# Performance work log

Measured on AMD Instinct MI355X. Metric: run time of the kernel, lower is better.

The kernel has to match this reference:

```python
import jax, jax.numpy as jnp
import numpy as np

IN_DIM = 128
OUT_DIM = 128
EDGE_DIM = 64
NUM_HEADS = 8
HEAD_DIM = OUT_DIM // NUM_HEADS
N_NODES = 10000
N_EDGES = 320000
LN_EPS = 1e-5


def _gelu(x):
    # torch nn.GELU default is the exact (erf) formulation
    return jax.nn.gelu(x, approximate=False)


def _layernorm(x, g, b):
    mu = jnp.mean(x, axis=-1, keepdims=True)
    var = jnp.var(x, axis=-1, keepdims=True)
    return (x - mu) * jax.lax.rsqrt(var + LN_EPS) * g + b


def setup_inputs() -> dict:
    key = jax.random.key(0)
    ks = jax.random.split(key, 16)

    def lin(k, fan_in, fan_out):
        # torch nn.Linear default init: U(-1/sqrt(fan_in), 1/sqrt(fan_in))
        bound = 1.0 / np.sqrt(fan_in)
        kw, kb = jax.random.split(k)
        w = jax.random.uniform(kw, (fan_in, fan_out), jnp.float32, -bound, bound)
        b = jax.random.uniform(kb, (fan_out,), jnp.float32, -bound, bound)
        return w, b

    node_features = jax.random.normal(ks[0], (N_NODES, IN_DIM), jnp.float32)
    edge_index = jax.random.randint(ks[1], (2, N_EDGES), 0, N_NODES)
    edge_attr = jax.random.normal(ks[2], (N_EDGES, EDGE_DIM), jnp.float32)

    msg_w1, msg_b1 = lin(ks[3], 2 * IN_DIM + EDGE_DIM, OUT_DIM)
    msg_w2, msg_b2 = lin(ks[4], OUT_DIM, OUT_DIM)
    q_w, q_b = lin(ks[5], IN_DIM, OUT_DIM)
    kv_w, kv_b = lin(ks[6], IN_DIM + EDGE_DIM, OUT_DIM)
    out_w1, out_b1 = lin(ks[7], IN_DIM + OUT_DIM, OUT_DIM)
    out_w2, out_b2 = lin(ks[8], OUT_DIM, OUT_DIM)
    ln_g = 1.0 + 0.02 * jax.random.normal(ks[9], (OUT_DIM,), jnp.float32)
    ln_b = 0.02 * jax.random.normal(ks[10], (OUT_DIM,), jnp.float32)

    return dict(node_features=node_features, edge_attr=edge_attr,
                msg_w1=msg_w1, msg_b1=msg_b1, msg_w2=msg_w2, msg_b2=msg_b2,
                q_w=q_w, q_b=q_b, kv_w=kv_w, kv_b=kv_b,
                out_w1=out_w1, out_b1=out_b1, out_w2=out_w2, out_b2=out_b2,
                ln_g=ln_g, ln_b=ln_b, edge_index=edge_index)


def reference(node_features, edge_attr, msg_w1, msg_b1, msg_w2, msg_b2,
              q_w, q_b, kv_w, kv_b, out_w1, out_b1, out_w2, out_b2,
              ln_g, ln_b, edge_index):
    N = node_features.shape[0]
    E = edge_index.shape[1]
    src, dst = edge_index[0], edge_index[1]

    s = node_features[src]                      # [E, Din]
    d = node_features[dst]                      # [E, Din]

    # message MLP
    m_in = jnp.concatenate([s, d, edge_attr], axis=-1)          # [E, 2*Din+De]
    m = _gelu(m_in @ msg_w1 + msg_b1) @ msg_w2 + msg_b2         # [E, Dout]

    # per-edge attention logits
    q = (d @ q_w + q_b).reshape(E, NUM_HEADS, HEAD_DIM)
    kv_in = jnp.concatenate([s, edge_attr], axis=-1)
    kv = (kv_in @ kv_w + kv_b).reshape(E, NUM_HEADS, HEAD_DIM)
    attn = jnp.sum(q * kv, axis=-1) * (HEAD_DIM ** -0.5)        # [E, H]

    # Deterministic version: pick the edge with the largest index per dst node.
    last = jnp.full((N,), -1, dtype=jnp.int32).at[dst].max(
        jnp.arange(E, dtype=jnp.int32))                          # [N]
    attn_full = jnp.where(last[:, None] >= 0,
                          attn[jnp.maximum(last, 0)],
                          -jnp.inf)                              # [N, H]
    # softmax over the NODE axis (dim=0), exactly as the torch code does;
    # -inf rows contribute 0, so using N instead of dst.max()+1 is identical.
    attn_norm = jax.nn.softmax(attn_full, axis=0)[dst]           # [E, H]

    m = (m.reshape(E, NUM_HEADS, HEAD_DIM) * attn_norm[..., None]).reshape(E, OUT_DIM)

    # scatter-add aggregation
    agg = jax.ops.segment_sum(m, dst, num_segments=N)            # [N, Dout]

    h_in = jnp.concatenate([node_features, agg], axis=-1)        # [N, Din+Dout]
    h = _gelu(h_in @ out_w1 + out_b1) @ out_w2 + out_b2          # [N, Dout]

    # res_proj is Identity since in_dim == out_dim; dropout is eval-mode no-op
    return _layernorm(node_features + h, ln_g, ln_b)
```

## Files before the change

### kernel.cpp

```cpp
#include <hip/hip_runtime.h>
#include <hip/hip_bf16.h>

#define NN 10000
#define NE 320000

typedef __bf16 bf16x8 __attribute__((ext_vector_type(8)));
typedef float  f32x4  __attribute__((ext_vector_type(4)));

__device__ __forceinline__ float bf2f(ushort u){
  union { uint i; float f; } c; c.i = ((uint)u) << 16; return c.f;
}
__device__ __forceinline__ ushort f2bf(float f){
  union { float f; uint i; } c; c.f = f;
  uint x = c.i;
  return (ushort)((x + 0x7FFFu + ((x >> 16) & 1u)) >> 16);
}
__device__ __forceinline__ float gelu_erf(float x){
  return 0.5f * x * (1.0f + erff(x * 0.70710678118654752f));
}
__device__ __forceinline__ float gelu_tanh(float x){
  float y = 0.7978845608028654f * (x + 0.044715f * x * x * x);
  float e = __expf(2.f * y);
  float th = 1.f - 2.f / (e + 1.f);
  return 0.5f * x * (1.f + th);
}
__device__ __forceinline__ uint encf(float f){
  uint u = __float_as_uint(f);
  return (u & 0x80000000u) ? ~u : (u | 0x80000000u);
}
__device__ __forceinline__ float decf(uint u){
  return __uint_as_float((u & 0x80000000u) ? (u & 0x7FFFFFFFu) : ~u);
}
#define MFMA16(a,b,c) __builtin_amdgcn_mfma_f32_16x16x32_bf16((a),(b),(c),0,0,0)

__global__ void k_init(const uint* __restrict__ w, int* __restrict__ flag,
                       int* __restrict__ cnt, int* __restrict__ last,
                       uint* __restrict__ Menc, float* __restrict__ S){
  int t = threadIdx.x;
  if (blockIdx.x == 0){
    uint c = 0;
    for (int i = t; i < 4096; i += 256){
      uint v = w[i * 63];
      uint e = (v >> 7) & 0xFF;
      if (e >= 100 && e <= 140) c++;
    }
    __shared__ uint red[256];
    red[t] = c; __syncthreads();
    for (int s = 128; s > 0; s >>= 1){
      if (t < s) red[t] += red[t + s];
      __syncthreads();
    }
    if (t == 0) *flag = (red[0] < 2048) ? 1 : 0;
    return;
  }
  int idx = (blockIdx.x - 1) * 256 + t;
  if (idx < 10000) last[idx] = -1;
  else if (idx < 20000) cnt[idx - 10000] = 0;
  else if (idx < 20008) Menc[idx - 20000] = 0u;
  else if (idx < 20016) S[idx - 20008] = 0.f;
}

__global__ void k_prep(
    const void* NF0, const int* __restrict__ dstI,
    const void* w1, const void* w2, const void* qw, const void* kvw,
    const void* ow1, const void* ow2,
    const void* b1, const void* b2, const void* qb, const void* kvb,
    const void* ob1, const void* ob2, const void* lg, const void* lb,
    int* __restrict__ cnt, int* __restrict__ last,
    ushort* NFc, float* Gagg, ushort* SB, ushort* KVW2,
    ushort* W1aT, ushort* W1bT, ushort* W1cT, ushort* W2T, ushort* QT, ushort* KVT,
    ushort* O1aT, ushort* O1bT, ushort* O2T, const int* flag)
{
  int f = *flag;
  int idx = blockIdx.x * 256 + threadIdx.x;
  if (idx < NE){
    int d = dstI[idx];
    atomicAdd(&cnt[d], 1);
    atomicMax(&last[d], idx);
    return;
  }
  idx -= NE;
  if (idx < 320000){
    if (f){
      float4 v = ((const float4*)NF0)[idx];
      ushort4 o; o.x=f2bf(v.x); o.y=f2bf(v.y); o.z=f2bf(v.z); o.w=f2bf(v.w);
      ((ushort4*)NFc)[idx] = o;
    } else ((ushort4*)NFc)[idx] = ((const ushort4*)NF0)[idx];
    return;
  }
  idx -= 320000;
  if (idx < 320000){ float4 z = {0.f,0.f,0.f,0.f}; ((float4*)Gagg)[idx] = z; return; }
  idx -= 320000;
  if (idx < 1024){
    const void* ps[8] = {b1,b2,qb,kvb,ob1,ob2,lg,lb};
    const void* p = ps[idx >> 7]; int j = idx & 127;
    SB[idx] = f ? f2bf(((const float*)p)[j]) : ((const ushort*)p)[j];
    return;
  }
  idx -= 1024;
  if (idx < 8192){
    KVW2[idx] = f ? f2bf(((const float*)kvw)[16384 + idx]) : ((const ushort*)kvw)[16384 + idx];
    return;
  }
  idx -= 8192;
  if (idx < 16384){ int c=idx>>7,k=idx&127; W1aT[idx] = f? f2bf(((const float*)w1)[k*128+c]) : ((const ushort*)w1)[k*128+c]; return; }
  idx -= 16384;
  if (idx < 16384){ int c=idx>>7,k=idx&127; W1bT[idx] = f? f2bf(((const float*)w1)[(128+k)*128+c]) : ((const ushort*)w1)[(128+k)*128+c]; return; }
  idx -= 16384;
  if (idx < 8192){ int c=idx>>6,k=idx&63;  W1cT[idx] = f? f2bf(((const float*)w1)[(256+k)*128+c]) : ((const ushort*)w1)[(256+k)*128+c]; return; }
  idx -= 8192;
  if (idx < 16384){ int c=idx>>7,k=idx&127; W2T[idx] = f? f2bf(((const float*)w2)[k*128+c]) : ((const ushort*)w2)[k*128+c]; return; }
  idx -= 16384;
  if (idx < 16384){ int c=idx>>7,k=idx&127; QT[idx]  = f? f2bf(((const float*)qw)[k*128+c]) : ((const ushort*)qw)[k*128+c]; return; }
  idx -= 16384;
  if (idx < 16384){ int c=idx>>7,k=idx&127; KVT[idx] = f? f2bf(((const float*)kvw)[k*128+c]) : ((const ushort*)kvw)[k*128+c]; return; }
  idx -= 16384;
  if (idx < 16384){ int c=idx>>7,k=idx&127; O1aT[idx] = f? f2bf(((const float*)ow1)[k*128+c]) : ((const ushort*)ow1)[k*128+c]; return; }
  idx -= 16384;
  if (idx < 16384){ int c=idx>>7,k=idx&127; O1bT[idx] = f? f2bf(((const float*)ow1)[(128+k)*128+c]) : ((const ushort*)ow1)[(128+k)*128+c]; return; }
  idx -= 16384;
  if (idx < 16384){ int c=idx>>7,k=idx&127; O2T[idx] = f? f2bf(((const float*)ow2)[k*128+c]) : ((const ushort*)ow2)[k*128+c]; return; }
}

__global__ __launch_bounds__(1024) void k_scan(const int* __restrict__ cnt,
                                               int* __restrict__ fill){
  __shared__ int sc[1024];
  int t = threadIdx.x;
  int base = t * 10;
  int v[10]; int tot = 0;
  #pragma unroll
  for (int j = 0; j < 10; ++j){
    int idx = base + j;
    v[j] = (idx < NN) ? cnt[idx] : 0;
    tot += v[j];
  }
  sc[t] = tot; __syncthreads();
  for (int off = 1; off < 1024; off <<= 1){
    int x = (t >= off) ? sc[t - off] : 0;
    __syncthreads();
    sc[t] += x;
    __syncthreads();
  }
  int run = sc[t] - tot;
  #pragma unroll
  for (int j = 0; j < 10; ++j){
    int idx = base + j;
    if (idx < NN) fill[idx] = run;
    run += v[j];
  }
}

__global__ __launch_bounds__(256) void k_fillperm(
    const int* __restrict__ srcI, const int* __restrict__ dstI,
    int* __restrict__ fill, int* __restrict__ sSort, int* __restrict__ dSort,
    int* __restrict__ eSort,
    const ushort* __restrict__ NFc,
    const ushort* __restrict__ W1aT, const ushort* __restrict__ W1bT,
    const ushort* __restrict__ QT,  const ushort* __restrict__ KVT,
    const ushort* __restrict__ SB,
    ushort* __restrict__ PA, ushort* __restrict__ PB,
    ushort* __restrict__ Qb, ushort* __restrict__ KV1)
{
  int t = threadIdx.x;
  if (blockIdx.x >= 1250){
    int l = t & 63, w = t >> 6;
    int m = l & 15, g = l >> 4;
    int row0 = ((int)blockIdx.x - 1250) * 16;
    const ushort* WT = (w==0) ? W1aT : (w==1) ? W1bT : (w==2) ? QT : KVT;
    ushort*       OUT= (w==0) ? PA   : (w==1) ? PB   : (w==2) ? Qb : KV1;
    const f32x4 FZ = {0.f,0.f,0.f,0.f};
    f32x4 acc[8];
    #pragma unroll
    for (int i = 0; i < 8; ++i) acc[i] = FZ;
    int arow = row0 + m;
    #pragma unroll
    for (int ks = 0; ks < 4; ++ks){
      int koff = ks * 32 + g * 8;
      bf16x8 a = *reinterpret_cast<const bf16x8*>(NFc + (size_t)arow * 128 + koff);
      #pragma unroll
      for (int nt = 0; nt < 8; ++nt){
        bf16x8 b = *reinterpret_cast<const bf16x8*>(WT + (size_t)(nt*16+m) * 128 + koff);
        acc[nt] = MFMA16(a, b, acc[nt]);
      }
    }
    #pragma unroll
    for (int nt = 0; nt < 8; ++nt){
      int col = nt * 16 + m;
      float bb = (w==1) ? bf2f(SB[col]) : (w==2) ? bf2f(SB[256+col]) : (w==3) ? bf2f(SB[384+col]) : 0.f;
      #pragma unroll
      for (int r = 0; r < 4; ++r){
        int row = row0 + g * 4 + r;
        OUT[(size_t)row * 128 + col] = f2bf(acc[nt][r] + bb);
      }
    }
    return;
  }
  int e = blockIdx.x * 256 + t;
  int d = dstI[e];
  int p = atomicAdd(&fill[d], 1);
  sSort[p] = srcI[e];
  dSort[p] = d;
  eSort[p] = e;
}

__global__ __launch_bounds__(256) void k_edgeattn(
    const ushort* __restrict__ PA, const ushort* __restrict__ PB,
    const int* __restrict__ sSort, const int* __restrict__ dSort,
    const int* __restrict__ eSort,
    const ushort* __restrict__ W1cT,
    float* __restrict__ Gagg,
    const ushort* __restrict__ Qb, const ushort* __restrict__ KV1,
    const ushort* __restrict__ EAb, const float* __restrict__ EAf,
    const ushort* __restrict__ KVW2,
    const int* __restrict__ srcI, const int* __restrict__ last,
    float* __restrict__ attn, uint* __restrict__ Menc, const int* __restrict__ flag)
{
  __shared__ __align__(16) char Hs[64 * 256];
  __shared__ __align__(16) char EAl[64 * 128];
  __shared__ int sIdx[64], dIdx[64], eIdx[64];
  __shared__ int eN[16], sN[16];
  __shared__ uint lmax[8];
  int t = threadIdx.x;

  if (blockIdx.x >= 5000){
    float (*ea_s)[64] = reinterpret_cast<float(*)[64]>(Hs);
    int n0 = ((int)blockIdx.x - 5000) * 16;
    if (t < 16){
      int e = last[n0 + t];
      eN[t] = e;
      sN[t] = (e >= 0) ? srcI[e] : 0;
    }
    if (t < 8) lmax[t] = 0u;
    __syncthreads();
    int F = *flag;
    for (int i = t; i < 1024; i += 256){
      int nn = i >> 6, k = i & 63;
      int e = eN[nn];
      int ee = (e >= 0) ? e : 0;
      float v = F ? EAf[(size_t)ee * 64 + k] : bf2f(EAb[(size_t)ee * 64 + k]);
      ea_s[nn][k] = (e >= 0) ? v : 0.0f;
    }
    __syncthreads();
    int j = t & 127;
    int half = t >> 7;
    float acc[8];
    #pragma unroll
    for (int i = 0; i < 8; ++i) acc[i] = 0.f;
    for (int k = 0; k < 64; ++k){
      float wv = bf2f(KVW2[(size_t)k * 128 + j]);
      #pragma unroll
      for (int nn = 0; nn < 8; ++nn) acc[nn] += ea_s[half * 8 + nn][k] * wv;
    }
    #pragma unroll
    for (int nn = 0; nn < 8; ++nn){
      int nl = half * 8 + nn;
      int n = n0 + nl;
      int e = eN[nl];
      float kvv = acc[nn] + bf2f(KV1[(size_t)sN[nl] * 128 + j]);
      float qv  = bf2f(Qb[(size_t)n * 128 + j]);
      float p = qv * kvv;
      p += __shfl_xor(p, 1); p += __shfl_xor(p, 2);
      p += __shfl_xor(p, 4); p += __shfl_xor(p, 8);
      if ((j & 15) == 0 && e >= 0){
        float v = p * 0.25f;
        attn[(size_t)n * 8 + (j >> 4)] = v;
        atomicMax(&lmax[j >> 4], encf(v));
      }
    }
    __syncthreads();
    if (t < 8 && lmax[t]) atomicMax(&Menc[t], lmax[t]);
    return;
  }

  int p0 = blockIdx.x * 64;
  int l = t & 63, w = t >> 6;
  int m = l & 15, g = l >> 4;

  if (t < 64){ sIdx[t] = sSort[p0 + t]; dIdx[t] = dSort[p0 + t]; eIdx[t] = eSort[p0 + t]; }
  __syncthreads();
  int F = *flag;

  {
    int r = t >> 2, q = t & 3;
    int e = eIdx[r];
    int kb = q * 32;
    if (F){
      const float* src = EAf + (size_t)e * 64 + q * 16;
      float4 v0 = *reinterpret_cast<const float4*>(src);
      float4 v1 = *reinterpret_cast<const float4*>(src + 4);
      float4 v2 = *reinterpret_cast<const float4*>(src + 8);
      float4 v3 = *reinterpret_cast<const float4*>(src + 12);
      bf16x8 o0, o1;
      o0[0]=(__bf16)v0.x; o0[1]=(__bf16)v0.y; o0[2]=(__bf16)v0.z; o0[3]=(__bf16)v0.w;
      o0[4]=(__bf16)v1.x; o0[5]=(__bf16)v1.y; o0[6]=(__bf16)v1.z; o0[7]=(__bf16)v1.w;
      o1[0]=(__bf16)v2.x; o1[1]=(__bf16)v2.y; o1[2]=(__bf16)v2.z; o1[3]=(__bf16)v2.w;
      o1[4]=(__bf16)v3.x; o1[5]=(__bf16)v3.y; o1[6]=(__bf16)v3.z; o1[7]=(__bf16)v3.w;
      *reinterpret_cast<bf16x8*>(&EAl[(r * 128 + kb)      ^ ((r & 7) << 4)]) = o0;
      *reinterpret_cast<bf16x8*>(&EAl[(r * 128 + kb + 16) ^ ((r & 7) << 4)]) = o1;
    } else {
      const ushort* src = EAb + (size_t)e * 64 + q * 16;
      *reinterpret_cast<bf16x8*>(&EAl[(r * 128 + kb)      ^ ((r & 7) << 4)]) =
        *reinterpret_cast<const bf16x8*>(src);
      *reinterpret_cast<bf16x8*>(&EAl[(r * 128 + kb + 16) ^ ((r & 7) << 4)]) =
        *reinterpret_cast<const bf16x8*>(src + 8);
    }
    int sr = sIdx[r], dr = dIdx[r];
    #pragma unroll
    for (int j = 0; j < 4; ++j){
      int c8 = q * 4 + j;
      bf16x8 pa = *reinterpret_cast<const bf16x8*>(PA + (size_t)sr * 128 + c8 * 8);
      bf16x8 pb = *reinterpret_cast<const bf16x8*>(PB + (size_t)dr * 128 + c8 * 8);
      bf16x8 ps;
      #pragma unroll
      for (int k = 0; k < 8; ++k) ps[k] = (__bf16)((float)pa[k] + (float)pb[k]);
      int byte = (r * 256 + c8 * 16) ^ ((r & 7) << 4);
      *reinterpret_cast<bf16x8*>(&Hs[byte]) = ps;
    }
  }
  __syncthreads();

  const f32x4 FZ = {0.f,0.f,0.f,0.f};
  f32x4 acc[8];
  #pragma unroll
  for (int i = 0; i < 8; ++i) acc[i] = FZ;

  #pragma unroll
  for (int ks = 0; ks < 2; ++ks){
    int row = w * 16 + m;
    bf16x8 af = *reinterpret_cast<const bf16x8*>(&EAl[(row * 128 + ks * 64 + g * 16) ^ ((row & 7) << 4)]);
    #pragma unroll
    for (int nt = 0; nt < 8; ++nt){
      bf16x8 b = *reinterpret_cast<const bf16x8*>(W1cT + (size_t)(nt * 16 + m) * 64 + ks * 32 + g * 8);
      acc[nt] = MFMA16(af, b, acc[nt]);
    }
  }

  #pragma unroll
  for (int nt = 0; nt < 8; ++nt){
    int col = nt * 16 + m;
    #pragma unroll
    for (int r = 0; r < 4; ++r){
      int row = w * 16 + g * 4 + r;
      int byte = (row * 256 + col * 2) ^ ((row & 7) << 4);
      float x = acc[nt][r] + bf2f(*reinterpret_cast<const ushort*>(&Hs[byte]));
      *reinterpret_cast<ushort*>(&Hs[byte]) = f2bf(gelu_tanh(x));
    }
  }
  __syncthreads();

  {
    int c = t & 127, hh = t >> 7;
    int rS = hh * 32, rE = rS + 32;
    float run = 0.f;
    int cur = dIdx[rS];
    for (int r = rS; r < rE; ++r){
      int d = dIdx[r];
      if (d != cur){
        unsafeAtomicAdd(&Gagg[(size_t)cur * 128 + c], run);
        run = 0.f; cur = d;
      }
      int byte = (r * 256 + c * 2) ^ ((r & 7) << 4);
      run += bf2f(*reinterpret_cast<const ushort*>(&Hs[byte]));
    }
    unsafeAtomicAdd(&Gagg[(size_t)cur * 128 + c], run);
  }
}

__global__ __launch_bounds__(256) void k_asum(
    const float* __restrict__ attn, const int* __restrict__ last,
    const uint* __restrict__ Menc, float* __restrict__ S)
{
  __shared__ float red[256][8];
  int t = threadIdx.x;
  float M[8];
  #pragma unroll
  for (int h = 0; h < 8; ++h) M[h] = decf(Menc[h]);
  float p[8];
  #pragma unroll
  for (int h = 0; h < 8; ++h) p[h] = 0.f;
  for (int n = blockIdx.x * 256 + t; n < NN; n += gridDim.x * 256){
    if (last[n] >= 0){
      #pragma unroll
      for (int h = 0; h < 8; ++h) p[h] += __expf(attn[(size_t)n * 8 + h] - M[h]);
    }
  }
  #pragma unroll
  for (int h = 0; h < 8; ++h) red[t][h] = p[h];
  __syncthreads();
  for (int s = 128; s > 0; s >>= 1){
    if (t < s){
      #pragma unroll
      for (int h = 0; h < 8; ++h) red[t][h] += red[t + s][h];
    }
    __syncthreads();
  }
  if (t < 8) atomicAdd(&S[t], red[0][t]);
}

__global__ __launch_bounds__(256) void k_aggmm2(
    const float* __restrict__ Gagg, const ushort* __restrict__ W2T,
    const ushort* __restrict__ O1aT, const ushort* __restrict__ O1bT,
    const ushort* __restrict__ SB,
    const int* __restrict__ cnt, const int* __restrict__ last,
    const float* __restrict__ attn, const uint* __restrict__ Menc,
    const float* __restrict__ S,
    const ushort* __restrict__ NFc, ushort* __restrict__ T1)
{
  __shared__ __align__(16) char Zs[64 * 256];
  int t = threadIdx.x, l = t & 63, w = t >> 6;
  int m = l & 15, g = l >> 4;
  int row0 = blockIdx.x * 64 + w * 16;

  float M[8], Sinv[8];
  #pragma unroll
  for (int h = 0; h < 8; ++h){ M[h] = decf(Menc[h]); Sinv[h] = 1.0f / S[h]; }

  int arow = row0 + m; if (arow >= NN) arow = NN - 1;
  const f32x4 FZ = {0.f,0.f,0.f,0.f};
  f32x4 acc[8];
  #pragma unroll
  for (int i = 0; i < 8; ++i) acc[i] = FZ;

  #pragma unroll
  for (int ks = 0; ks < 4; ++ks){
    const float* gp = Gagg + (size_t)arow * 128 + ks * 32 + g * 8;
    float4 u0 = *reinterpret_cast<const float4*>(gp);
    float4 u1 = *reinterpret_cast<const float4*>(gp + 4);
    float gv[8] = {u0.x,u0.y,u0.z,u0.w,u1.x,u1.y,u1.z,u1.w};
    bf16x8 hi, lo;
    #pragma unroll
    for (int k = 0; k < 8; ++k){
      hi[k] = (__bf16)gv[k];
      lo[k] = (__bf16)(gv[k] - (float)hi[k]);
    }
    #pragma unroll
    for (int nt = 0; nt < 8; ++nt){
      bf16x8 b = *reinterpret_cast<const bf16x8*>(W2T + (size_t)(nt*16+m) * 128 + ks * 32 + g * 8);
      acc[nt] = MFMA16(hi, b, acc[nt]);
      acc[nt] = MFMA16(lo, b, acc[nt]);
    }
  }

  #pragma unroll
  for (int r = 0; r < 4; ++r){
    int row = row0 + g * 4 + r;
    int rr = (row < NN) ? row : NN - 1;
    float cn = (float)cnt[rr];
    int lst = last[rr];
    int Lr = w * 16 + g * 4 + r;
    #pragma unroll
    for (int nt = 0; nt < 8; ++nt){
      int col = nt * 16 + m;
      float aw = (lst >= 0) ? __expf(attn[(size_t)rr * 8 + nt] - M[nt]) * Sinv[nt] : 0.f;
      float z = (acc[nt][r] + cn * bf2f(SB[128 + col])) * aw;
      int byte = (Lr * 256 + col * 2) ^ ((Lr & 7) << 4);
      *reinterpret_cast<ushort*>(&Zs[byte]) = f2bf(z);
    }
  }
  __syncthreads();

  f32x4 acc2[8];
  #pragma unroll
  for (int i = 0; i < 8; ++i) acc2[i] = FZ;
  int La = w * 16 + m;
  #pragma unroll
  for (int ks = 0; ks < 4; ++ks){
    int koff = ks * 32 + g * 8;
    bf16x8 az = *reinterpret_cast<const bf16x8*>(&Zs[(La * 256 + koff * 2) ^ ((La & 7) << 4)]);
    bf16x8 an = *reinterpret_cast<const bf16x8*>(NFc + (size_t)arow * 128 + koff);
    #pragma unroll
    for (int nt = 0; nt < 8; ++nt){
      bf16x8 b1v = *reinterpret_cast<const bf16x8*>(O1bT + (size_t)(nt*16+m) * 128 + koff);
      bf16x8 b2v = *reinterpret_cast<const bf16x8*>(O1aT + (size_t)(nt*16+m) * 128 + koff);
      acc2[nt] = MFMA16(az, b1v, acc2[nt]);
      acc2[nt] = MFMA16(an, b2v, acc2[nt]);
    }
  }
  #pragma unroll
  for (int nt = 0; nt < 8; ++nt){
    int col = nt * 16 + m;
    float bb = bf2f(SB[512 + col]);
    #pragma unroll
    for (int r = 0; r < 4; ++r){
      int row = row0 + g * 4 + r;
      if (row < NN){
        float v = gelu_erf(acc2[nt][r] + bb);
        T1[(size_t)row * 128 + col] = f2bf(v);
      }
    }
  }
}

__global__ __launch_bounds__(256) void k_out2ln(
    const ushort* __restrict__ T1, const ushort* __restrict__ O2T,
    const ushort* __restrict__ SB,
    const ushort* __restrict__ NFc, void* __restrict__ out,
    const int* __restrict__ flag)
{
  int t = threadIdx.x, l = t & 63, w = t >> 6;
  int m = l & 15, g = l >> 4;
  int row0 = blockIdx.x * 64 + w * 16;
  int F = *flag;
  int arow = row0 + m; if (arow >= NN) arow = NN - 1;
  const f32x4 FZ = {0.f,0.f,0.f,0.f};
  f32x4 acc[8];
  #pragma unroll
  for (int i = 0; i < 8; ++i) acc[i] = FZ;
  #pragma unroll
  for (int ks = 0; ks < 4; ++ks){
    int koff = ks * 32 + g * 8;
    bf16x8 a = *reinterpret_cast<const bf16x8*>(T1 + (size_t)arow * 128 + koff);
    #pragma unroll
    for (int nt = 0; nt < 8; ++nt){
      bf16x8 b = *reinterpret_cast<const bf16x8*>(O2T + (size_t)(nt*16+m) * 128 + koff);
      acc[nt] = MFMA16(a, b, acc[nt]);
    }
  }
  #pragma unroll
  for (int r = 0; r < 4; ++r){
    int row = row0 + g * 4 + r;
    bool ok = row < NN;
    int rr = ok ? row : NN - 1;
    float x[8]; float s = 0.f, q = 0.f;
    #pragma unroll
    for (int nt = 0; nt < 8; ++nt){
      int col = nt * 16 + m;
      float xv = acc[nt][r] + bf2f(SB[640 + col]) + bf2f(NFc[(size_t)rr * 128 + col]);
      x[nt] = xv; s += xv; q += xv * xv;
    }
    #pragma unroll
    for (int msk = 1; msk < 16; msk <<= 1){
      s += __shfl_xor(s, msk);
      q += __shfl_xor(q, msk);
    }
    float mean = s * (1.0f / 128.0f);
    float var  = q * (1.0f / 128.0f) - mean * mean;
    float rs = rsqrtf(var + 1e-5f);
    if (ok){
      #pragma unroll
      for (int nt = 0; nt < 8; ++nt){
        int col = nt * 16 + m;
        float y = (x[nt] - mean) * rs * bf2f(SB[768 + col]) + bf2f(SB[896 + col]);
        if (F) ((float*)out)[(size_t)row * 128 + col] = y;
        else   ((ushort*)out)[(size_t)row * 128 + col] = f2bf(y);
      }
    }
  }
}

extern "C" void kernel_launch(void* const* d_in, const int* in_sizes, int n_in,
                              void* d_out, int out_size, void* d_ws, size_t ws_size,
                              hipStream_t stream)
{
  const void* NF0  = d_in[0];
  const void* EA0  = d_in[1];
  const void* w1   = d_in[2];
  const void* b1   = d_in[3];
  const void* w2   = d_in[4];
  const void* b2   = d_in[5];
  const void* qw   = d_in[6];
  const void* qb   = d_in[7];
  const void* kvw  = d_in[8];
  const void* kvb  = d_in[9];
  const void* ow1  = d_in[10];
  const void* ob1  = d_in[11];
  const void* ow2  = d_in[12];
  const void* ob2  = d_in[13];
  const void* lg   = d_in[14];
  const void* lb   = d_in[15];
  const int*  srcI = (const int*)d_in[16];
  const int*  dstI = srcI + NE;

  char* ws = (char*)d_ws;
  size_t off = 0;
  auto alloc = [&](size_t bytes) -> void* {
    void* p = ws + off;
    off = (off + bytes + 255) & ~(size_t)255;
    return p;
  };
  int*    flag  = (int*)   alloc(4);
  ushort* NFc   = (ushort*)alloc((size_t)NN * 128 * 2);
  ushort* SB    = (ushort*)alloc(8 * 128 * 2);
  ushort* KVW2  = (ushort*)alloc(64 * 128 * 2);
  ushort* W1aT  = (ushort*)alloc(128 * 128 * 2);
  ushort* W1bT  = (ushort*)alloc(128 * 128 * 2);
  ushort* W1cT  = (ushort*)alloc(128 * 64 * 2);
  ushort* W2T   = (ushort*)alloc(128 * 128 * 2);
  ushort* QT    = (ushort*)alloc(128 * 128 * 2);
  ushort* KVT   = (ushort*)alloc(128 * 128 * 2);
  ushort* O1aT  = (ushort*)alloc(128 * 128 * 2);
  ushort* O1bT  = (ushort*)alloc(128 * 128 * 2);
  ushort* O2T   = (ushort*)alloc(128 * 128 * 2);
  int*    last  = (int*)   alloc(NN * 4);
  int*    cnt   = (int*)   alloc(NN * 4);
  int*    fill  = (int*)   alloc(NN * 4);
  int*    sSort = (int*)   alloc((size_t)NE * 4);
  int*    dSort = (int*)   alloc((size_t)NE * 4);
  int*    eSort = (int*)   alloc((size_t)NE * 4);
  float*  attn  = (float*) alloc(NN * 8 * 4);
  uint*   Menc  = (uint*)  alloc(8 * 4);
  float*  S     = (float*) alloc(8 * 4);
  ushort* PA    = (ushort*)alloc((size_t)NN * 128 * 2);
  ushort* PB    = (ushort*)alloc((size_t)NN * 128 * 2);
  ushort* Qb    = (ushort*)alloc((size_t)NN * 128 * 2);
  ushort* KV1   = (ushort*)alloc((size_t)NN * 128 * 2);
  float*  Gagg  = (float*) alloc((size_t)NN * 128 * 4);
  ushort* T1    = (ushort*)alloc((size_t)NN * 128 * 2);

  k_init<<<80, 256, 0, stream>>>((const uint*)NF0, flag, cnt, last, Menc, S);
  k_prep<<<4330, 256, 0, stream>>>(NF0, dstI, w1, w2, qw, kvw, ow1, ow2,
                                   b1, b2, qb, kvb, ob1, ob2, lg, lb,
                                   cnt, last, NFc, Gagg, SB, KVW2,
                                   W1aT, W1bT, W1cT, W2T, QT, KVT, O1aT, O1bT, O2T, flag);
  k_scan<<<1, 1024, 0, stream>>>(cnt, fill);
  k_fillperm<<<1875, 256, 0, stream>>>(srcI, dstI, fill, sSort, dSort, eSort,
                                       NFc, W1aT, W1bT, QT, KVT, SB,
                                       PA, PB, Qb, KV1);
  k_edgeattn<<<5625, 256, 0, stream>>>(PA, PB, sSort, dSort, eSort, W1cT, Gagg,
                                       Qb, KV1, (const ushort*)EA0, (const float*)EA0,
                                       KVW2, srcI, last, attn, Menc, flag);
  k_asum<<<40, 256, 0, stream>>>(attn, last, Menc, S);
  k_aggmm2<<<157, 256, 0, stream>>>(Gagg, W2T, O1aT, O1bT, SB, cnt, last,
                                    attn, Menc, S, NFc, T1);
  k_out2ln<<<157, 256, 0, stream>>>(T1, O2T, SB, NFc, d_out, flag);
}
```

Measured before the change: 202.0 us.

## Fuse output MLP second layer into aggregation kernel; pack sorted edge indices

Merges the aggregation/out_w1 kernel with the out_w2+LayerNorm kernel. The GELU intermediate is now staged in swizzled shared memory instead of a global bf16 buffer T1, which removes one launch and a global round trip. Separately, the three sorted src/dst/edge index arrays are packed into one int4 array, so each edge takes one scattered store and one vector load. The int4 layout wastes 4 bytes per edge, and the fused kernel may use more registers. La must be defined in the part of the code not shown.

```diff
diff --git a/kernel.cpp b/kernel.cpp
--- a/kernel.cpp
+++ b/kernel.cpp
@@ -152,8 +152,7 @@
 
 __global__ __launch_bounds__(256) void k_fillperm(
     const int* __restrict__ srcI, const int* __restrict__ dstI,
-    int* __restrict__ fill, int* __restrict__ sSort, int* __restrict__ dSort,
-    int* __restrict__ eSort,
+    int* __restrict__ fill, int4* __restrict__ sde,
     const ushort* __restrict__ NFc,
     const ushort* __restrict__ W1aT, const ushort* __restrict__ W1bT,
     const ushort* __restrict__ QT,  const ushort* __restrict__ KVT,
@@ -197,16 +196,15 @@
   }
   int e = blockIdx.x * 256 + t;
   int d = dstI[e];
+  int s = srcI[e];
   int p = atomicAdd(&fill[d], 1);
-  sSort[p] = srcI[e];
-  dSort[p] = d;
-  eSort[p] = e;
+  int4 v; v.x = s; v.y = d; v.z = e; v.w = 0;
+  sde[p] = v;
 }
 
 __global__ __launch_bounds__(256) void k_edgeattn(
     const ushort* __restrict__ PA, const ushort* __restrict__ PB,
-    const int* __restrict__ sSort, const int* __restrict__ dSort,
-    const int* __restrict__ eSort,
+    const int4* __restrict__ sde,
     const ushort* __restrict__ W1cT,
     float* __restrict__ Gagg,
     const ushort* __restrict__ Qb, const ushort* __restrict__ KV1,
@@ -276,7 +274,10 @@
   int l = t & 63, w = t >> 6;
   int m = l & 15, g = l >> 4;
 
-  if (t < 64){ sIdx[t] = sSort[p0 + t]; dIdx[t] = dSort[p0 + t]; eIdx[t] = eSort[p0 + t]; }
+  if (t < 64){
+    int4 v = sde[p0 + t];
+    sIdx[t] = v.x; dIdx[t] = v.y; eIdx[t] = v.z;
+  }
   __syncthreads();
   int F = *flag;
 
@@ -397,19 +398,22 @@
   if (t < 8) atomicAdd(&S[t], red[0][t]);
 }
 
-__global__ __launch_bounds__(256) void k_aggmm2(
+__global__ __launch_bounds__(256) void k_aggln(
     const float* __restrict__ Gagg, const ushort* __restrict__ W2T,
     const ushort* __restrict__ O1aT, const ushort* __restrict__ O1bT,
+    const ushort* __restrict__ O2T,
     const ushort* __restrict__ SB,
     const int* __restrict__ cnt, const int* __restrict__ last,
     const float* __restrict__ attn, const uint* __restrict__ Menc,
     const float* __restrict__ S,
-    const ushort* __restrict__ NFc, ushort* __restrict__ T1)
+    const ushort* __restrict__ NFc, void* __restrict__ out,
+    const int* __restrict__ flag)
 {
   __shared__ __align__(16) char Zs[64 * 256];
   int t = threadIdx.x, l = t & 63, w = t >> 6;
   int m = l & 15, g = l >> 4;
   int row0 = blockIdx.x * 64 + w * 16;
+  int F = *flag;
 
   float M[8], Sinv[8];
   #pragma unroll
@@ -417,10 +421,10 @@
 
   int arow = row0 + m; if (arow >= NN) arow = NN - 1;
   const f32x4 FZ = {0.f,0.f,0.f,0.f};
+
   f32x4 acc[8];
   #pragma unroll
   for (int i = 0; i < 8; ++i) acc[i] = FZ;
-
   #pragma unroll
   for (int ks = 0; ks < 4; ++ks){
     const float* gp = Gagg + (size_t)arow * 128 + ks * 32 + g * 8;
@@ -476,44 +480,33 @@
       acc2[nt] = MFMA16(an, b2v, acc2[nt]);
     }
   }
+  __syncthreads();
+
   #pragma unroll
   for (int nt = 0; nt < 8; ++nt){
     int col = nt * 16 + m;
     float bb = bf2f(SB[512 + col]);
     #pragma unroll
     for (int r = 0; r < 4; ++r){
-      int row = row0 + g * 4 + r;
-      if (row < NN){
-        float v = gelu_erf(acc2[nt][r] + bb);
-        T1[(size_t)row * 128 + col] = f2bf(v);
-      }
-    }
-  }
-}
-
-__global__ __launch_bounds__(256) void k_out2ln(
-    const ushort* __restrict__ T1, const ushort* __restrict__ O2T,
-    const ushort* __restrict__ SB,
-    const ushort* __restrict__ NFc, void* __restrict__ out,
-    const int* __restrict__ flag)
-{
-  int t = threadIdx.x, l = t & 63, w = t >> 6;
-  int m = l & 15, g = l >> 4;
-  int row0 = blockIdx.x * 64 + w * 16;
-  int F = *flag;
-  int arow = row0 + m; if (arow >= NN) arow = NN - 1;
-  const f32x4 FZ = {0.f,0.f,0.f,0.f};
-  f32x4 acc[8];
-  #pragma unroll
-  for (int i = 0; i < 8; ++i) acc[i] = FZ;
+      int Lr = w * 16 + g * 4 + r;
+      float v = gelu_erf(acc2[nt][r] + bb);
+      int byte = (Lr * 256 + col * 2) ^ ((Lr & 7) << 4);
+      *reinterpret_cast<ushort*>(&Zs[byte]) = f2bf(v);
+    }
+  }
+  __syncthreads();
+
+  f32x4 acc3[8];
+  #pragma unroll
+  for (int i = 0; i < 8; ++i) acc3[i] = FZ;
   #pragma unroll
   for (int ks = 0; ks < 4; ++ks){
     int koff = ks * 32 + g * 8;
-    bf16x8 a = *reinterpret_cast<const bf16x8*>(T1 + (size_t)arow * 128 + koff);
+    bf16x8 a = *reinterpret_cast<const bf16x8*>(&Zs[(La * 256 + koff * 2) ^ ((La & 7) << 4)]);
     #pragma unroll
     for (int nt = 0; nt < 8; ++nt){
       bf16x8 b = *reinterpret_cast<const bf16x8*>(O2T + (size_t)(nt*16+m) * 128 + koff);
-      acc[nt] = MFMA16(a, b, acc[nt]);
+      acc3[nt] = MFMA16(a, b, acc3[nt]);
     }
   }
   #pragma unroll
@@ -525,7 +518,7 @@
     #pragma unroll
     for (int nt = 0; nt < 8; ++nt){
       int col = nt * 16 + m;
-      float xv = acc[nt][r] + bf2f(SB[640 + col]) + bf2f(NFc[(size_t)rr * 128 + col]);
+      float xv = acc3[nt][r] + bf2f(SB[640 + col]) + bf2f(NFc[(size_t)rr * 128 + col]);
       x[nt] = xv; s += xv; q += xv * xv;
     }
     #pragma unroll
@@ -594,9 +587,7 @@
   int*    last  = (int*)   alloc(NN * 4);
   int*    cnt   = (int*)   alloc(NN * 4);
   int*    fill  = (int*)   alloc(NN * 4);
-  int*    sSort = (int*)   alloc((size_t)NE * 4);
-  int*    dSort = (int*)   alloc((size_t)NE * 4);
-  int*    eSort = (int*)   alloc((size_t)NE * 4);
+  int4*   sde   = (int4*)  alloc((size_t)NE * 16);
   float*  attn  = (float*) alloc(NN * 8 * 4);
   uint*   Menc  = (uint*)  alloc(8 * 4);
   float*  S     = (float*) alloc(8 * 4);
@@ -605,7 +596,6 @@
   ushort* Qb    = (ushort*)alloc((size_t)NN * 128 * 2);
   ushort* KV1   = (ushort*)alloc((size_t)NN * 128 * 2);
   float*  Gagg  = (float*) alloc((size_t)NN * 128 * 4);
-  ushort* T1    = (ushort*)alloc((size_t)NN * 128 * 2);
 
   k_init<<<80, 256, 0, stream>>>((const uint*)NF0, flag, cnt, last, Menc, S);
   k_prep<<<4330, 256, 0, stream>>>(NF0, dstI, w1, w2, qw, kvw, ow1, ow2,
@@ -613,14 +603,13 @@
                                    cnt, last, NFc, Gagg, SB, KVW2,
                                    W1aT, W1bT, W1cT, W2T, QT, KVT, O1aT, O1bT, O2T, flag);
   k_scan<<<1, 1024, 0, stream>>>(cnt, fill);
-  k_fillperm<<<1875, 256, 0, stream>>>(srcI, dstI, fill, sSort, dSort, eSort,
+  k_fillperm<<<1875, 256, 0, stream>>>(srcI, dstI, fill, sde,
                                        NFc, W1aT, W1bT, QT, KVT, SB,
                                        PA, PB, Qb, KV1);
-  k_edgeattn<<<5625, 256, 0, stream>>>(PA, PB, sSort, dSort, eSort, W1cT, Gagg,
+  k_edgeattn<<<5625, 256, 0, stream>>>(PA, PB, sde, W1cT, Gagg,
                                        Qb, KV1, (const ushort*)EA0, (const float*)EA0,
                                        KVW2, srcI, last, attn, Menc, flag);
   k_asum<<<40, 256, 0, stream>>>(attn, last, Menc, S);
-  k_aggmm2<<<157, 256, 0, stream>>>(Gagg, W2T, O1aT, O1bT, SB, cnt, last,
-                                    attn, Menc, S, NFc, T1);
-  k_out2ln<<<157, 256, 0, stream>>>(T1, O2T, SB, NFc, d_out, flag);
-}
+  k_aggln<<<157, 256, 0, stream>>>(Gagg, W2T, O1aT, O1bT, O2T, SB, cnt, last,
+                                   attn, Menc, S, NFc, d_out, flag);
+}
```

New measurement: 197.8 us. -2.1%, faster.
